# Performance work log

Hardware: AMD Instinct MI355X
Metric: run time of the kernel (lower is better)

Reference implementation:

```python
import jax, jax.numpy as jnp
import numpy as np

B, S, D, H = 2, 2048, 1024, 16
HEAD_DIM = D // H
THETA = 10000.0


def setup_inputs() -> dict:
    key = jax.random.key(0)
    kx, kq, kk, kv, ko = jax.random.split(key, 5)
    w_scale = jnp.float32(D ** -0.5)  # keep logits O(1)
    return {
        "x": jax.random.normal(kx, (B, S, D), dtype=jnp.float32),
        "WQ": jax.random.normal(kq, (D, D), dtype=jnp.float32) * w_scale,
        "WK": jax.random.normal(kk, (D, D), dtype=jnp.float32) * w_scale,
        "WV": jax.random.normal(kv, (D, D), dtype=jnp.float32) * w_scale,
        "WO": jax.random.normal(ko, (D, D), dtype=jnp.float32) * w_scale,
        "token_positions": jnp.arange(S, dtype=jnp.int32),
    }


def _rope(x, pos, theta):
    # x: [B, H, S, dh]; pos: [S]. Interleaved (even, odd) pair rotation.
    dh = x.shape[-1]
    inv_freq = theta ** (-jnp.arange(0, dh, 2, dtype=jnp.float32) / dh)  # [dh/2]
    ang = pos.astype(jnp.float32)[:, None] * inv_freq                    # [S, dh/2]
    cos, sin = jnp.cos(ang), jnp.sin(ang)
    x1, x2 = x[..., 0::2], x[..., 1::2]
    r1 = x1 * cos - x2 * sin
    r2 = x1 * sin + x2 * cos
    return jnp.stack([r1, r2], axis=-1).reshape(x.shape)


def reference(x, WQ, WK, WV, WO, token_positions):
    Bs, Ss, Dm = x.shape
    dh = Dm // H
    # QKV projections (Linear with no bias, y = x @ W.T), split heads -> [B,H,S,dh]
    q = (x @ WQ.T).reshape(Bs, Ss, H, dh).transpose(0, 2, 1, 3)
    k = (x @ WK.T).reshape(Bs, Ss, H, dh).transpose(0, 2, 1, 3)
    v = (x @ WV.T).reshape(Bs, Ss, H, dh).transpose(0, 2, 1, 3)
    q = _rope(q, token_positions, THETA)
    k = _rope(k, token_positions, THETA)
    scores = jnp.einsum("bhqd,bhkd->bhqk", q, k) * jnp.float32(dh ** -0.5)
    causal = jnp.tril(jnp.ones((Ss, Ss), dtype=bool))
    scores = jnp.where(causal, scores, jnp.finfo(scores.dtype).min)
    attn = jax.nn.softmax(scores, axis=-1)
    out = jnp.einsum("bhqk,bhkd->bhqd", attn, v)
    out = out.transpose(0, 2, 1, 3).reshape(Bs, Ss, Dm)
    return out @ WO.T
```

## Files before the change

kernel.cpp:

```cpp
#include <hip/hip_runtime.h>
#include <hip/hip_bf16.h>


#define S_LEN 2048
#define NEG_SENT -30000.0f

typedef __attribute__((ext_vector_type(8))) short short8;
typedef __attribute__((ext_vector_type(4))) float f32x4;
typedef unsigned int u32;
typedef unsigned short u16;

static __device__ __forceinline__ float bf2f(u16 u) {
  union { u32 i; float f; } v; v.i = ((u32)u) << 16; return v.f;
}
static __device__ __forceinline__ u16 f2bf(float f) {
  union { float f; u32 i; } v; v.f = f;
  u32 u = v.i;
  u32 r = (u + 0x7fffu + ((u >> 16) & 1u)) >> 16;
  return (u16)r;
}
static __device__ __forceinline__ u32 cvtpk(float a, float b) {
  u32 r;
  asm("v_cvt_pk_bf16_f32 %0, %1, %2" : "=v"(r) : "v"(a), "v"(b));
  return r;
}

static __device__ __forceinline__ void glds16(const void* g, void* l) {
  __builtin_amdgcn_global_load_lds((const __attribute__((address_space(1))) u32*)g,
                                   (__attribute__((address_space(3))) u32*)l, 16, 0, 0);
}

__global__ void convert_kernel(const float* __restrict__ x, const float* __restrict__ wq,
                               const float* __restrict__ wk, const float* __restrict__ wv,
                               const float* __restrict__ wo, const int* __restrict__ pos,
                               u16* __restrict__ xb, u16* __restrict__ wb,
                               float2* __restrict__ tab) {
  const int stride = gridDim.x * blockDim.x;
  for (int i = blockIdx.x * blockDim.x + threadIdx.x; i < 2162688; i += stride) {
    if (i >= 2097152) {
      int e = i - 2097152;
      int s = e >> 5, ip = e & 31;
      float p = (float)pos[s];
      float ang = p * __builtin_exp2f((float)ip * -0.41524101186f);
      float sn, cs;
      sincosf(ang, &sn, &cs);
      tab[e] = make_float2(cs, sn);
      continue;
    }
    const float* src; u16* dst; int off;
    if (i < 1048576) { src = x; dst = xb; off = i; }
    else {
      int j = i - 1048576;
      int widx = j >> 18;
      off = j & 262143;
      src = (widx == 0) ? wq : (widx == 1) ? wk : (widx == 2) ? wv : wo;
      dst = wb + (size_t)widx * 1048576;
    }
    float4 v = ((const float4*)src)[off];
    ushort4 o;
    o.x = f2bf(v.x); o.y = f2bf(v.y); o.z = f2bf(v.z); o.w = f2bf(v.w);
    ((ushort4*)dst)[off] = o;
  }
}

template <int OUTMODE>
__global__ __launch_bounds__(256, 2) void gemm_bt(const u16* __restrict__ A,
                                                  const u16* __restrict__ B,
                                                  u16* __restrict__ o0, u16* __restrict__ o1,
                                                  u16* __restrict__ o2, float* __restrict__ oF,
                                                  const float2* __restrict__ tab, int K) {
  __shared__ __align__(16) u16 AsBs[2 * 128 * 64];
  u16* const As = AsBs;
  u16* const Bs = AsBs + 128 * 64;
  const int tid = threadIdx.x, w = tid >> 6, l = tid & 63, l15 = l & 15, l4 = l >> 4;
  const int wr = w >> 1, wc = w & 1;
  const int lid = blockIdx.y * gridDim.x + blockIdx.x;
  const int xcd = lid & 7;
  const int jj2 = lid >> 3;
  const int mrows = gridDim.y >> 3;
  const int m0 = (xcd * mrows + jj2 / gridDim.x) << 7;
  const int n0 = (jj2 % gridDim.x) << 7;
  const int r = tid >> 3;
  const int swcol = ((tid & 7) << 4) ^ ((r & 7) << 4);
  const char* Ag = (const char*)A + (((size_t)(m0 + r) * K) << 1) + swcol;
  const char* Bg = (const char*)B + (((size_t)(n0 + r) * K) << 1) + swcol;
  char* AsW = (char*)As + (w << 10);
  char* BsW = (char*)Bs + (w << 10);
  const size_t rowskip = ((size_t)32 * K) << 1;
  f32x4 acc[4][4] = {};
  for (int k0 = 0; k0 < K; k0 += 64) {
    __syncthreads();
    const size_t kb = (size_t)k0 << 1;
#pragma unroll
    for (int i = 0; i < 4; i++) {
      glds16(Ag + kb + (size_t)i * rowskip, AsW + i * 4096);
      glds16(Bg + kb + (size_t)i * rowskip, BsW + i * 4096);
    }
    __syncthreads();
#pragma unroll
    for (int kk = 0; kk < 2; kk++) {
      short8 a[4], b[4];
#pragma unroll
      for (int m = 0; m < 4; m++) {
        int row = (wr << 6) + (m << 4) + l15;
        a[m] = *(const short8*)((const char*)As + row * 128 +
                                (((kk << 6) + (l4 << 4)) ^ ((row & 7) << 4)));
      }
#pragma unroll
      for (int n = 0; n < 4; n++) {
        int row = (wc << 6) + (n << 4) + l15;
        b[n] = *(const short8*)((const char*)Bs + row * 128 +
                                (((kk << 6) + (l4 << 4)) ^ ((row & 7) << 4)));
      }
#pragma unroll
      for (int m = 0; m < 4; m++)
#pragma unroll
        for (int n = 0; n < 4; n++)
          acc[m][n] = __builtin_amdgcn_mfma_f32_16x16x32_bf16(a[m], b[n], acc[m][n], 0, 0, 0);
    }
  }
  if (OUTMODE == 0 && n0 >= 2048) {
    __syncthreads();
    u16* T = AsBs;
#pragma unroll
    for (int m = 0; m < 4; m++)
#pragma unroll
      for (int n = 0; n < 4; n++) {
        int ct = (wc << 6) + (n << 4) + l15;
#pragma unroll
        for (int j = 0; j < 4; j++) {
          int rt = (wr << 6) + (m << 4) + (l4 << 2) + j;
          T[rt * 128 + (ct ^ (((rt >> 6) & 1) << 1))] = f2bf(acc[m][n][j]);
        }
      }
    __syncthreads();
    const int d = tid >> 1, sh = tid & 1;
    const int dr = d ^ (sh << 1);
    const int bb = m0 >> 11;
    const int colv = (n0 & 1023) + d;
    const int row = (((bb << 4) | (colv >> 6)) << 6) | (colv & 63);
    u16* dst = o2 + ((size_t)row << 11) + (m0 & (S_LEN - 1)) + (sh << 6);
#pragma unroll
    for (int k8 = 0; k8 < 8; k8++) {
      u16 tmp[8];
#pragma unroll
      for (int e = 0; e < 8; e++) tmp[e] = T[((sh << 6) + (k8 << 3) + e) * 128 + dr];
      *(uint4*)(dst + (k8 << 3)) = *(const uint4*)tmp;
    }
    return;
  }
#pragma unroll
  for (int m = 0; m < 4; m++) {
    int grow_b = m0 + (wr << 6) + (m << 4) + (l4 << 2);
#pragma unroll
    for (int n = 0; n < 4; n++) {
      int gcol = n0 + (wc << 6) + (n << 4) + l15;
      if (OUTMODE == 1) {
#pragma unroll
        for (int j = 0; j < 4; j++)
          oF[((size_t)(grow_b + j) << 10) + gcol] = acc[m][n][j];
      } else {
        const float qscale = (gcol < 1024) ? 0.125f * 1.44269504089f : 1.f;
        u16* base = (gcol < 1024) ? o0 : o1;
        const int col = gcol & 1023;
        const int d = col & 63;
        const float sgn = (d & 1) ? 1.f : -1.f;
        const int ip = d >> 1;
#pragma unroll
        for (int j = 0; j < 4; j++) {
          int grow = grow_b + j;
          float v = acc[m][n][j] * qscale;
          float pv = __shfl_xor(v, 1, 64);
          float2 cssn = tab[((grow & (S_LEN - 1)) << 5) + ip];
          base[((size_t)grow << 10) + col] = f2bf(v * cssn.x + pv * cssn.y * sgn);
        }
      }
    }
  }
}

__global__ __launch_bounds__(512, 1) void attn_kernel(const u16* __restrict__ Q,
                                                      const u16* __restrict__ K,
                                                      const u16* __restrict__ Vt,
                                                      u16* __restrict__ O) {
  extern __shared__ __align__(16) char smem[];
  const int tid = threadIdx.x, w = tid >> 6, l = tid & 63, l15 = l & 15, g = l >> 4;
  const int grp = w >> 2, w4 = w & 3;
  const int i = blockIdx.x;
  const int xcd = i & 7, slot = i >> 3;
  const int bh = ((slot >> 3) << 3) | xcd;
  const int p = slot & 7;
  const int b = bh >> 4, h = bh & 15;
  const int swz = (l15 & 7) << 4;

  const int gt = tid & 255;
  const int r = gt >> 3;
  const int swc = ((gt & 7) << 4) ^ ((r & 7) << 4);
  const char* Kg = (const char*)K + ((size_t)(b * S_LEN + r) << 11) + (h << 7) + swc;
  const char* Vg = (const char*)Vt + ((size_t)((bh << 6) + r) << 12) + swc;
  char* const KsG = smem + (grp << 16);
  char* const VsG = smem + (grp << 16) + 32768;
  char* const Pw = smem + 131072 + (w << 11);
  float* const oMrg = (float*)smem;
  float* const lMrg = (float*)(smem + 131072);

#define STAGE2(PI, BSEL)                                            \
  do {                                                              \
    char* kd = KsG + ((BSEL) << 14) + (w4 << 10);                   \
    char* vd = VsG + ((BSEL) << 14) + (w4 << 10);                   \
    const char* ks = Kg + ((size_t)(PI) << 18);                     \
    const char* vs = Vg + ((PI) << 8);                              \
    glds16(ks, kd);                                                 \
    glds16(ks + (32 << 11), kd + 4096);                             \
    glds16(ks + (64 << 11), kd + 8192);                             \
    glds16(ks + (96 << 11), kd + 12288);                            \
    glds16(vs, vd);                                                 \
    glds16(vs + ((size_t)32 << 12), vd + 4096);                     \
    glds16(vs + 128, vd + 8192);                                    \
    glds16(vs + 128 + ((size_t)32 << 12), vd + 12288);              \
  } while (0)

  auto run_qt = [&](int qt) {
    const int q0 = qt << 7;
    const int nr = (qt + 2) >> 1;

    short8 aQ[2][2];
    {
      const int qrow0 = q0 + (w4 << 5) + l15;
      const u16* qp = Q + (((size_t)(b * S_LEN + qrow0)) << 10) + (h << 6) + (g << 3);
      aQ[0][0] = *(const short8*)qp;
      aQ[0][1] = *(const short8*)(qp + 32);
      aQ[1][0] = *(const short8*)(qp + (16 << 10));
      aQ[1][1] = *(const short8*)(qp + (16 << 10) + 32);
    }
    f32x4 o[2][4] = {};
    float l_r[2] = {0.f, 0.f};

    auto subtile = [&](int t, const char* Kbuf, const char* Vbuf, bool domask) {
      f32x4 s[2][4] = {};
#pragma unroll
      for (int kk = 0; kk < 2; ++kk) {
        short8 aK[4];
#pragma unroll
        for (int n = 0; n < 4; ++n) {
          int row = (n << 4) + l15;
          aK[n] = *(const short8*)(Kbuf + row * 128 + (((kk << 6) + (g << 4)) ^ swz));
        }
        __builtin_amdgcn_s_setprio(1);
#pragma unroll
        for (int n = 0; n < 4; ++n) {
          s[0][n] = __builtin_amdgcn_mfma_f32_16x16x32_bf16(aK[n], aQ[0][kk], s[0][n], 0, 0, 0);
          s[1][n] = __builtin_amdgcn_mfma_f32_16x16x32_bf16(aK[n], aQ[1][kk], s[1][n], 0, 0, 0);
        }
        __builtin_amdgcn_s_setprio(0);
      }
      if (domask) {
#pragma unroll
        for (int qs = 0; qs < 2; ++qs) {
          int qg = q0 + (w4 << 5) + (qs << 4) + l15;
#pragma unroll
          for (int n = 0; n < 4; ++n)
#pragma unroll
            for (int jj = 0; jj < 4; ++jj) {
              int key = (t << 6) + (n << 4) + (g << 2) + jj;
              if (key > qg) s[qs][n][jj] = NEG_SENT;
            }
        }
      }
      short8 aP[2][2];
#pragma unroll
      for (int qs = 0; qs < 2; ++qs) {
        float rs = 0.f;
        u32 pk[8];
#pragma unroll
        for (int n = 0; n < 4; ++n) {
          float p0 = __builtin_exp2f(s[qs][n][0]);
          float p1 = __builtin_exp2f(s[qs][n][1]);
          float p2 = __builtin_exp2f(s[qs][n][2]);
          float p3 = __builtin_exp2f(s[qs][n][3]);
          rs += (p0 + p1) + (p2 + p3);
          pk[2 * n] = cvtpk(p0, p1);
          pk[2 * n + 1] = cvtpk(p2, p3);
        }
        l_r[qs] += rs;
        char* pr = Pw + l15 * 128;
#pragma unroll
        for (int n = 0; n < 4; ++n) {
          uint2 pv;
          pv.x = pk[2 * n];
          pv.y = pk[2 * n + 1];
          *(uint2*)(pr + (((n << 5) + (g << 3)) ^ swz)) = pv;
        }
#pragma unroll
        for (int kk = 0; kk < 2; ++kk)
          aP[qs][kk] = *(const short8*)(pr + (((kk << 6) + (g << 4)) ^ swz));
      }
#pragma unroll
      for (int kk = 0; kk < 2; ++kk) {
        int co = (kk << 6) + (g << 4);
        __builtin_amdgcn_s_setprio(1);
#pragma unroll
        for (int nd = 0; nd < 4; ++nd) {
          int row = (nd << 4) + l15;
          short8 bV = *(const short8*)(Vbuf + row * 128 + (co ^ swz));
          o[0][nd] = __builtin_amdgcn_mfma_f32_16x16x32_bf16(aP[0][kk], bV, o[0][nd], 0, 0, 0);
          o[1][nd] = __builtin_amdgcn_mfma_f32_16x16x32_bf16(aP[1][kk], bV, o[1][nd], 0, 0, 0);
        }
        __builtin_amdgcn_s_setprio(0);
      }
    };

    if (grp <= qt) STAGE2(grp, 0);
    __syncthreads();

    for (int rr = 0; rr < nr; ++rr) {
      const int bsel = rr & 1;
      const int pi = 2 * rr + grp;
      if (pi + 2 <= qt) STAGE2(pi + 2, bsel ^ 1);
      if (pi <= qt) {
        const char* Kb0 = KsG + (bsel << 14);
        const char* Vb0 = VsG + (bsel << 14);
        const bool dm = (pi == qt);
        subtile(2 * pi, Kb0, Vb0, dm);
        subtile(2 * pi + 1, Kb0 + 8192, Vb0 + 8192, dm);
      }
      __syncthreads();
    }

    if (grp == 1) {
      float* ob = oMrg + (w4 << 11);
#pragma unroll
      for (int qs = 0; qs < 2; ++qs)
#pragma unroll
        for (int nd = 0; nd < 4; ++nd)
          *(f32x4*)(ob + (((qs << 2) | nd) << 8) + (l << 2)) = o[qs][nd];
      float* lb = lMrg + (w4 << 7);
      lb[l] = l_r[0];
      lb[64 + l] = l_r[1];
    }
    __syncthreads();
    if (grp == 0) {
      float* ob = oMrg + (w4 << 11);
      float* lb = lMrg + (w4 << 7);
#pragma unroll
      for (int qs = 0; qs < 2; ++qs) {
        float lsum = l_r[qs] + lb[(qs << 6) + l];
        lsum += __shfl_xor(lsum, 16);
        lsum += __shfl_xor(lsum, 32);
        float linv = 1.f / lsum;
        f32x4 oB[4];
#pragma unroll
        for (int nd = 0; nd < 4; ++nd)
          oB[nd] = *(const f32x4*)(ob + (((qs << 2) | nd) << 8) + (l << 2));
#pragma unroll
        for (int jj = 0; jj < 4; ++jj) {
          float lo = __shfl(linv, (g << 2) + jj, 16);
          int qg = q0 + (w4 << 5) + (qs << 4) + (g << 2) + jj;
          u16* orow = O + (((size_t)(b * S_LEN + qg)) << 10) + (h << 6) + l15;
#pragma unroll
          for (int nd = 0; nd < 4; ++nd)
            orow[nd << 4] = f2bf((o[qs][nd][jj] + oB[nd][jj]) * lo);
        }
      }
    }
    __syncthreads();
  };

  run_qt(p);
  run_qt(15 - p);
#undef STAGE2
}

extern "C" void kernel_launch(void* const* d_in, const int* in_sizes, int n_in,
                              void* d_out, int out_size, void* d_ws, size_t ws_size,
                              hipStream_t stream) {
  (void)in_sizes; (void)n_in; (void)out_size; (void)ws_size;
  const float* x = (const float*)d_in[0];
  const float* wq = (const float*)d_in[1];
  const float* wk = (const float*)d_in[2];
  const float* wv = (const float*)d_in[3];
  const float* wo = (const float*)d_in[4];
  const int* pos = (const int*)d_in[5];
  char* ws = (char*)d_ws;
  u16* xb = (u16*)ws;
  u16* wb = (u16*)(ws + ((size_t)8 << 20));
  u16* Qb = (u16*)(ws + ((size_t)16 << 20));
  u16* Kb = (u16*)(ws + ((size_t)24 << 20));
  u16* Vtg = (u16*)(ws + ((size_t)32 << 20));
  u16* Ab = (u16*)(ws + ((size_t)40 << 20));
  float* out = (float*)d_out;
  float2* tab = (float2*)d_out;

  convert_kernel<<<2112, 256, 0, stream>>>(x, wq, wk, wv, wo, pos, xb, wb, tab);
  dim3 g1(24, 32);
  gemm_bt<0><<<g1, 256, 0, stream>>>(xb, wb, Qb, Kb, Vtg, nullptr, tab, 1024);
  attn_kernel<<<256, 512, 147456, stream>>>(Qb, Kb, Vtg, Ab);
  dim3 g3(8, 32);
  gemm_bt<1><<<g3, 256, 0, stream>>>(Ab, wb + (size_t)3 * 1048576, nullptr, nullptr, nullptr,
                                     out, nullptr, 1024);
}
```

Before: 102.4 us.

## Split attention key loop across three wave groups with 64-key tiles

```diff
diff --git a/kernel.cpp b/kernel.cpp
--- a/kernel.cpp
+++ b/kernel.cpp
@@ -179,13 +179,13 @@
   }
 }
 
-__global__ __launch_bounds__(512, 1) void attn_kernel(const u16* __restrict__ Q,
+__global__ __launch_bounds__(768, 3) void attn_kernel(const u16* __restrict__ Q,
                                                       const u16* __restrict__ K,
                                                       const u16* __restrict__ Vt,
                                                       u16* __restrict__ O) {
   extern __shared__ __align__(16) char smem[];
   const int tid = threadIdx.x, w = tid >> 6, l = tid & 63, l15 = l & 15, g = l >> 4;
-  const int grp = w >> 2, w4 = w & 3;
+  const int grp = tid >> 8, w4 = (tid >> 6) & 3;
   const int i = blockIdx.x;
   const int xcd = i & 7, slot = i >> 3;
   const int bh = ((slot >> 3) << 3) | xcd;
@@ -198,31 +198,29 @@
   const int swc = ((gt & 7) << 4) ^ ((r & 7) << 4);
   const char* Kg = (const char*)K + ((size_t)(b * S_LEN + r) << 11) + (h << 7) + swc;
   const char* Vg = (const char*)Vt + ((size_t)((bh << 6) + r) << 12) + swc;
-  char* const KsG = smem + (grp << 16);
-  char* const VsG = smem + (grp << 16) + 32768;
-  char* const Pw = smem + 131072 + (w << 11);
-  float* const oMrg = (float*)smem;
-  float* const lMrg = (float*)(smem + 131072);
-
-#define STAGE2(PI, BSEL)                                            \
+  char* const KsG = smem + grp * 32768;
+  char* const VsG = smem + grp * 32768 + 16384;
+  char* const Pw = smem + 98304 + (w << 11);
+  float* const oMrg1 = (float*)smem;
+  float* const oMrg2 = (float*)(smem + 32768);
+  float* const lMrg = (float*)(smem + 122880);
+
+#define STAGE(T, BSEL)                                              \
   do {                                                              \
-    char* kd = KsG + ((BSEL) << 14) + (w4 << 10);                   \
-    char* vd = VsG + ((BSEL) << 14) + (w4 << 10);                   \
-    const char* ks = Kg + ((size_t)(PI) << 18);                     \
-    const char* vs = Vg + ((PI) << 8);                              \
+    char* kd = KsG + ((BSEL) << 13) + (w4 << 10);                   \
+    char* vd = VsG + ((BSEL) << 13) + (w4 << 10);                   \
+    const char* ks = Kg + ((size_t)(T) << 17);                      \
+    const char* vs = Vg + ((T) << 7);                               \
     glds16(ks, kd);                                                 \
     glds16(ks + (32 << 11), kd + 4096);                             \
-    glds16(ks + (64 << 11), kd + 8192);                             \
-    glds16(ks + (96 << 11), kd + 12288);                            \
     glds16(vs, vd);                                                 \
     glds16(vs + ((size_t)32 << 12), vd + 4096);                     \
-    glds16(vs + 128, vd + 8192);                                    \
-    glds16(vs + 128 + ((size_t)32 << 12), vd + 12288);              \
   } while (0)
 
   auto run_qt = [&](int qt) {
     const int q0 = qt << 7;
-    const int nr = (qt + 2) >> 1;
+    const int nt = (qt + 1) << 1;
+    const int nr = (nt + 2) / 3;
 
     short8 aQ[2][2];
     {
@@ -310,48 +308,48 @@
       }
     };
 
-    if (grp <= qt) STAGE2(grp, 0);
+    if (grp < nt) STAGE(grp, 0);
     __syncthreads();
 
     for (int rr = 0; rr < nr; ++rr) {
       const int bsel = rr & 1;
-      const int pi = 2 * rr + grp;
-      if (pi + 2 <= qt) STAGE2(pi + 2, bsel ^ 1);
-      if (pi <= qt) {
-        const char* Kb0 = KsG + (bsel << 14);
-        const char* Vb0 = VsG + (bsel << 14);
-        const bool dm = (pi == qt);
-        subtile(2 * pi, Kb0, Vb0, dm);
-        subtile(2 * pi + 1, Kb0 + 8192, Vb0 + 8192, dm);
+      const int t = 3 * rr + grp;
+      if (t + 3 < nt) STAGE(t + 3, bsel ^ 1);
+      if (t < nt) {
+        subtile(t, KsG + (bsel << 13), VsG + (bsel << 13), t >= nt - 2);
       }
       __syncthreads();
     }
 
-    if (grp == 1) {
-      float* ob = oMrg + (w4 << 11);
+    if (grp >= 1) {
+      float* ob = ((grp == 1) ? oMrg1 : oMrg2) + (w4 << 11);
 #pragma unroll
       for (int qs = 0; qs < 2; ++qs)
 #pragma unroll
         for (int nd = 0; nd < 4; ++nd)
           *(f32x4*)(ob + (((qs << 2) | nd) << 8) + (l << 2)) = o[qs][nd];
-      float* lb = lMrg + (w4 << 7);
+      float* lb = lMrg + ((grp - 1) << 9) + (w4 << 7);
       lb[l] = l_r[0];
       lb[64 + l] = l_r[1];
     }
     __syncthreads();
     if (grp == 0) {
-      float* ob = oMrg + (w4 << 11);
-      float* lb = lMrg + (w4 << 7);
+      float* ob1 = oMrg1 + (w4 << 11);
+      float* ob2 = oMrg2 + (w4 << 11);
+      float* lb1 = lMrg + (w4 << 7);
+      float* lb2 = lMrg + 512 + (w4 << 7);
 #pragma unroll
       for (int qs = 0; qs < 2; ++qs) {
-        float lsum = l_r[qs] + lb[(qs << 6) + l];
+        float lsum = l_r[qs] + lb1[(qs << 6) + l] + lb2[(qs << 6) + l];
         lsum += __shfl_xor(lsum, 16);
         lsum += __shfl_xor(lsum, 32);
         float linv = 1.f / lsum;
-        f32x4 oB[4];
-#pragma unroll
-        for (int nd = 0; nd < 4; ++nd)
-          oB[nd] = *(const f32x4*)(ob + (((qs << 2) | nd) << 8) + (l << 2));
+        f32x4 oB1[4], oB2[4];
+#pragma unroll
+        for (int nd = 0; nd < 4; ++nd) {
+          oB1[nd] = *(const f32x4*)(ob1 + (((qs << 2) | nd) << 8) + (l << 2));
+          oB2[nd] = *(const f32x4*)(ob2 + (((qs << 2) | nd) << 8) + (l << 2));
+        }
 #pragma unroll
         for (int jj = 0; jj < 4; ++jj) {
           float lo = __shfl(linv, (g << 2) + jj, 16);
@@ -359,7 +357,7 @@
           u16* orow = O + (((size_t)(b * S_LEN + qg)) << 10) + (h << 6) + l15;
 #pragma unroll
           for (int nd = 0; nd < 4; ++nd)
-            orow[nd << 4] = f2bf((o[qs][nd][jj] + oB[nd][jj]) * lo);
+            orow[nd << 4] = f2bf((o[qs][nd][jj] + oB1[nd][jj] + oB2[nd][jj]) * lo);
         }
       }
     }
@@ -368,7 +366,7 @@
 
   run_qt(p);
   run_qt(15 - p);
-#undef STAGE2
+#undef STAGE
 }
 
 extern "C" void kernel_launch(void* const* d_in, const int* in_sizes, int n_in,
@@ -394,7 +392,7 @@
   convert_kernel<<<2112, 256, 0, stream>>>(x, wq, wk, wv, wo, pos, xb, wb, tab);
   dim3 g1(24, 32);
   gemm_bt<0><<<g1, 256, 0, stream>>>(xb, wb, Qb, Kb, Vtg, nullptr, tab, 1024);
-  attn_kernel<<<256, 512, 147456, stream>>>(Qb, Kb, Vtg, Ab);
+  attn_kernel<<<256, 768, 126976, stream>>>(Qb, Kb, Vtg, Ab);
   dim3 g3(8, 32);
   gemm_bt<1><<<g3, 256, 0, stream>>>(Ab, wb + (size_t)3 * 1048576, nullptr, nullptr, nullptr,
                                      out, nullptr, 1024);
```

Result: no change. 102.2 us (-0.2%).

## Permute K rows in shared memory so P stays in registers for PV MFMA

Applied to the files above, without the earlier changes.

```diff
diff --git a/kernel.cpp b/kernel.cpp
--- a/kernel.cpp
+++ b/kernel.cpp
@@ -195,12 +195,12 @@
 
   const int gt = tid & 255;
   const int r = gt >> 3;
+  const int kr = ((r & 28) << 1) | (r & 3);
   const int swc = ((gt & 7) << 4) ^ ((r & 7) << 4);
-  const char* Kg = (const char*)K + ((size_t)(b * S_LEN + r) << 11) + (h << 7) + swc;
+  const char* Kg = (const char*)K + ((size_t)(b * S_LEN + kr) << 11) + (h << 7) + swc;
   const char* Vg = (const char*)Vt + ((size_t)((bh << 6) + r) << 12) + swc;
   char* const KsG = smem + (grp << 16);
   char* const VsG = smem + (grp << 16) + 32768;
-  char* const Pw = smem + 131072 + (w << 11);
   float* const oMrg = (float*)smem;
   float* const lMrg = (float*)(smem + 131072);
 
@@ -211,9 +211,9 @@
     const char* ks = Kg + ((size_t)(PI) << 18);                     \
     const char* vs = Vg + ((PI) << 8);                              \
     glds16(ks, kd);                                                 \
-    glds16(ks + (32 << 11), kd + 4096);                             \
+    glds16(ks + (4 << 11), kd + 4096);                              \
     glds16(ks + (64 << 11), kd + 8192);                             \
-    glds16(ks + (96 << 11), kd + 12288);                            \
+    glds16(ks + (68 << 11), kd + 12288);                            \
     glds16(vs, vd);                                                 \
     glds16(vs + ((size_t)32 << 12), vd + 4096);                     \
     glds16(vs + 128, vd + 8192);                                    \
@@ -262,7 +262,7 @@
           for (int n = 0; n < 4; ++n)
 #pragma unroll
             for (int jj = 0; jj < 4; ++jj) {
-              int key = (t << 6) + (n << 4) + (g << 2) + jj;
+              int key = (t << 6) + ((n & 1) << 5) + (g << 3) + ((n >> 1) << 2) + jj;
               if (key > qg) s[qs][n][jj] = NEG_SENT;
             }
         }
@@ -270,30 +270,27 @@
       short8 aP[2][2];
 #pragma unroll
       for (int qs = 0; qs < 2; ++qs) {
+        float p_[4][4];
         float rs = 0.f;
-        u32 pk[8];
 #pragma unroll
         for (int n = 0; n < 4; ++n) {
-          float p0 = __builtin_exp2f(s[qs][n][0]);
-          float p1 = __builtin_exp2f(s[qs][n][1]);
-          float p2 = __builtin_exp2f(s[qs][n][2]);
-          float p3 = __builtin_exp2f(s[qs][n][3]);
-          rs += (p0 + p1) + (p2 + p3);
-          pk[2 * n] = cvtpk(p0, p1);
-          pk[2 * n + 1] = cvtpk(p2, p3);
+#pragma unroll
+          for (int jj = 0; jj < 4; ++jj) {
+            p_[n][jj] = __builtin_exp2f(s[qs][n][jj]);
+            rs += p_[n][jj];
+          }
         }
         l_r[qs] += rs;
-        char* pr = Pw + l15 * 128;
-#pragma unroll
-        for (int n = 0; n < 4; ++n) {
-          uint2 pv;
-          pv.x = pk[2 * n];
-          pv.y = pk[2 * n + 1];
-          *(uint2*)(pr + (((n << 5) + (g << 3)) ^ swz)) = pv;
-        }
-#pragma unroll
-        for (int kk = 0; kk < 2; ++kk)
-          aP[qs][kk] = *(const short8*)(pr + (((kk << 6) + (g << 4)) ^ swz));
+#pragma unroll
+        for (int kk = 0; kk < 2; ++kk) {
+          union { u32 u[4]; short8 v; } wd;
+#pragma unroll
+          for (int wi = 0; wi < 4; ++wi) {
+            const int nw = ((wi >> 1) << 1) | kk;
+            wd.u[wi] = cvtpk(p_[nw][(wi & 1) * 2], p_[nw][(wi & 1) * 2 + 1]);
+          }
+          aP[qs][kk] = wd.v;
+        }
       }
 #pragma unroll
       for (int kk = 0; kk < 2; ++kk) {
@@ -394,7 +391,7 @@
   convert_kernel<<<2112, 256, 0, stream>>>(x, wq, wk, wv, wo, pos, xb, wb, tab);
   dim3 g1(24, 32);
   gemm_bt<0><<<g1, 256, 0, stream>>>(xb, wb, Qb, Kb, Vtg, nullptr, tab, 1024);
-  attn_kernel<<<256, 512, 147456, stream>>>(Qb, Kb, Vtg, Ab);
+  attn_kernel<<<256, 512, 135168, stream>>>(Qb, Kb, Vtg, Ab);
   dim3 g3(8, 32);
   gemm_bt<1><<<g3, 256, 0, stream>>>(Ab, wb + (size_t)3 * 1048576, nullptr, nullptr, nullptr,
                                      out, nullptr, 1024);
```

After: 100.7 us. Within noise of the previous version (-1.6%).
